# Optimization experiments

Hardware: AMD Instinct MI355X
Metric: run time of the kernel (lower is better)

## Reference

```python
import jax, jax.numpy as jnp
import numpy as np

BN_EPS = 1e-5


def setup_inputs() -> dict:
    key = jax.random.key(0)
    k1, k2, k3, k4 = jax.random.split(key, 4)
    B, H, W, C = 2, 256, 256, 256
    x = jax.random.normal(k1, (B, H, W, C), dtype=jnp.float32)
    # 1x1 conv weights (bias=False), randomly initialized each forward in the original
    w_down = jax.random.normal(k2, (16, C), dtype=jnp.float32) * (1.0 / np.sqrt(C))
    w_up = jax.random.normal(k3, (C, 16), dtype=jnp.float32) * (1.0 / np.sqrt(16))
    w_final = jax.random.normal(k4, (C, 2 * C), dtype=jnp.float32) * (1.0 / np.sqrt(2 * C))
    return {"x": x, "w_down": w_down, "w_up": w_up, "w_final": w_final}


def reference(x, w_down, w_up, w_final):
    # x: [B, H, W, C] -> NCHW
    x = jnp.transpose(x, (0, 3, 1, 2))  # [B, C, H, W]
    B, C, H, W = x.shape
    # fresh BatchNorm2d in training mode: batch stats, weight=1, bias=0
    mean = jnp.mean(x, axis=(0, 2, 3), keepdims=True)
    var = jnp.var(x, axis=(0, 2, 3), keepdims=True)  # biased variance
    xn = (x - mean) * jax.lax.rsqrt(var + BN_EPS)  # [B, C, H, W]
    # relu -> sigmoid
    a = jax.nn.sigmoid(jax.nn.relu(xn))
    # down-channel 1x1 conv: C -> 16
    y = jnp.einsum('oc,bchw->bohw', w_down, a)  # [B, 16, H, W]
    f = y.reshape(B, 16, H * W)  # flattened per-sample [16, HW]
    # channel self-attention; NOTE: source bug reuses Gram of sample 0 for sample 1
    G0 = f[0] @ f[0].T  # [16, 16]
    out0 = G0 @ f[0]    # [16, HW]
    out1 = G0 @ f[1]    # [16, HW]  (faithful to xcam4b = Dot(xcam3a, xcam1b))
    xcam4 = jnp.stack([out0, out1], axis=0).reshape(B, 16, H, W)
    # up-channel 1x1 conv: 16 -> C
    up = jnp.einsum('co,bohw->bchw', w_up, xcam4)  # [B, C, H, W]
    cat = jnp.concatenate([xn, up], axis=1)  # [B, 2C, H, W]
    # final down-channel 1x1 conv: 2C -> C
    out = jnp.einsum('oc,bchw->bohw', w_final, cat)  # [B, C, H, W]
    return out
```

## Files before the change

kernel.cpp:

```cpp
#include <hip/hip_runtime.h>
#include <stdint.h>

typedef __attribute__((ext_vector_type(8))) short bf16x8;
typedef __attribute__((ext_vector_type(4))) float f32x4;

#define CC 256
#define HWP 65536

__device__ __forceinline__ unsigned short f2bf(float f) {
    union { float f; unsigned int u; } v; v.f = f;
    unsigned int u = v.u;
    return (unsigned short)((u + 0x7fffu + ((u >> 16) & 1u)) >> 16);
}
__device__ __forceinline__ unsigned int f2bf2(float lo, float hi) {
    return (unsigned)f2bf(lo) | ((unsigned)f2bf(hi) << 16);
}
__device__ __forceinline__ float sigm_relu(float xn) {
    float xr = fmaxf(xn, 0.f);
    float e = __expf(-xr);
    return __builtin_amdgcn_rcpf(1.f + e);
}

__global__ __launch_bounds__(512, 8) void k1_part(const float* __restrict__ x,
                                                  float* __restrict__ part) {
    __shared__ float red[8][520];
    const int t = threadIdx.x, bid = blockIdx.x;
    const int c4 = (t & 63) * 4, po = t >> 6;
    const float* xp = x + ((size_t)(bid * 256 + po)) * CC + c4;
    f32x4 s = {0.f, 0.f, 0.f, 0.f}, q = {0.f, 0.f, 0.f, 0.f};
    #pragma unroll 8
    for (int p = 0; p < 32; ++p) {
        f32x4 v = *(const f32x4*)(xp + (size_t)p * 8 * CC);
        s += v; q += v * v;
    }
    *(f32x4*)&red[po][c4] = s;
    *(f32x4*)&red[po][256 + c4] = q;
    __syncthreads();
    float r = 0.f;
    #pragma unroll
    for (int po2 = 0; po2 < 8; ++po2) r += red[po2][t];
    part[bid * 512 + t] = r;
}

__global__ __launch_bounds__(256) void k2a_red(const float* __restrict__ part,
                                               float* __restrict__ p2) {
    int t = threadIdx.x, r = blockIdx.x;
    float s = 0.f, q = 0.f;
    #pragma unroll
    for (int i = 0; i < 16; ++i) {
        s += part[(size_t)(r * 16 + i) * 512 + t];
        q += part[(size_t)(r * 16 + i) * 512 + 256 + t];
    }
    p2[r * 512 + t] = s;
    p2[r * 512 + 256 + t] = q;
}

__global__ __launch_bounds__(256) void k2b_stats(const float* __restrict__ p2,
                                                 float* __restrict__ mg,
                                                 float* __restrict__ ig) {
    int c = threadIdx.x;
    float s = 0.f, q = 0.f;
    #pragma unroll
    for (int r = 0; r < 32; ++r) { s += p2[r * 512 + c]; q += p2[r * 512 + 256 + c]; }
    float mean = s * (1.f / 131072.f);
    float var  = q * (1.f / 131072.f) - mean * mean;
    mg[c] = mean;
    ig[c] = rsqrtf(var + 1e-5f);
}

__global__ __launch_bounds__(512) void k3_gram(const float* __restrict__ x,
                                               const float* __restrict__ wd,
                                               const float* __restrict__ mg,
                                               const float* __restrict__ ig,
                                               float* __restrict__ gpart) {
    __shared__ uint4 apack[2048];
    __shared__ float y_s[2][16][68];
    const int t = threadIdx.x;
    const int w = t >> 6, lm = t & 15, lk = (t >> 4) & 3;
    const int h = w & 1, ntile = w >> 1;
    uint4 wfrag[4];
    #pragma unroll
    for (int kt = 0; kt < 4; ++kt) {
        const int kbr = h * 16 + kt * 4 + lk;
        f32x4 wa = *(const f32x4*)(wd + lm * 256 + kbr * 8);
        f32x4 wb = *(const f32x4*)(wd + lm * 256 + kbr * 8 + 4);
        wfrag[kt] = (uint4){f2bf2(wa[0], wa[1]), f2bf2(wa[2], wa[3]),
                            f2bf2(wb[0], wb[1]), f2bf2(wb[2], wb[3])};
    }
    const int kb = t & 31, c0 = kb * 8, nb = t >> 5;
    f32x4 m0 = *(const f32x4*)(mg + c0), m1 = *(const f32x4*)(mg + c0 + 4);
    f32x4 i0 = *(const f32x4*)(ig + c0), i1 = *(const f32x4*)(ig + c0 + 4);
    const float mm[8] = {m0[0],m0[1],m0[2],m0[3],m1[0],m1[1],m1[2],m1[3]};
    const float ii[8] = {i0[0],i0[1],i0[2],i0[3],i1[0],i1[1],i1[2],i1[3]};
    const int o1 = t >> 4, o2 = t & 15;
    float g = 0.f;
    for (int st = 0; st < 4; ++st) {
        const float* xb = x + ((size_t)(blockIdx.x * 256 + st * 64 + nb)) * CC + c0;
        #pragma unroll
        for (int rep = 0; rep < 4; ++rep) {
            int n = rep * 16 + nb;
            const float* xp = xb + (size_t)rep * 16 * CC;
            f32x4 v0 = *(const f32x4*)xp;
            f32x4 v1 = *(const f32x4*)(xp + 4);
            float vv[8] = {v0[0],v0[1],v0[2],v0[3],v1[0],v1[1],v1[2],v1[3]};
            unsigned aw[4];
            #pragma unroll
            for (int hh = 0; hh < 4; ++hh) {
                float a0 = sigm_relu((vv[2*hh]   - mm[2*hh])   * ii[2*hh]);
                float a1 = sigm_relu((vv[2*hh+1] - mm[2*hh+1]) * ii[2*hh+1]);
                aw[hh] = f2bf2(a0, a1);
            }
            apack[kb * 64 + (n ^ kb)] = (uint4){aw[0], aw[1], aw[2], aw[3]};
        }
        __syncthreads();
        f32x4 accY = {0.f, 0.f, 0.f, 0.f};
        #pragma unroll
        for (int kt = 0; kt < 4; ++kt) {
            const int kbr = h * 16 + kt * 4 + lk;
            uint4 u = apack[kbr * 64 + ((ntile * 16 + lm) ^ kbr)];
            accY = __builtin_amdgcn_mfma_f32_16x16x32_bf16(*(bf16x8*)&wfrag[kt], *(bf16x8*)&u, accY, 0, 0, 0);
        }
        #pragma unroll
        for (int i = 0; i < 4; ++i) y_s[h][lk * 4 + i][ntile * 16 + lm] = accY[i];
        __syncthreads();
        if (t < 256) {
            #pragma unroll
            for (int p4 = 0; p4 < 16; ++p4) {
                f32x4 a0 = *(const f32x4*)&y_s[0][o1][p4 * 4];
                f32x4 a1 = *(const f32x4*)&y_s[1][o1][p4 * 4];
                f32x4 b0 = *(const f32x4*)&y_s[0][o2][p4 * 4];
                f32x4 b1 = *(const f32x4*)&y_s[1][o2][p4 * 4];
                f32x4 ya = a0 + a1, yb = b0 + b1;
                g += ya[0]*yb[0] + ya[1]*yb[1] + ya[2]*yb[2] + ya[3]*yb[3];
            }
        }
        __syncthreads();
    }
    if (t < 256) gpart[blockIdx.x * 256 + t] = g;
}

__global__ __launch_bounds__(256) void k4_R(const float* __restrict__ gpart,
                                            const float* __restrict__ wd,
                                            float* __restrict__ Rg) {
    __shared__ float G_s[256];
    const int t = threadIdx.x;
    float g = 0.f;
    #pragma unroll 8
    for (int i = 0; i < 256; ++i) g += gpart[i * 256 + t];
    G_s[t] = g;
    __syncthreads();
    #pragma unroll
    for (int o = 0; o < 16; ++o) {
        float r = 0.f;
        #pragma unroll
        for (int o2 = 0; o2 < 16; ++o2) r += G_s[o * 16 + o2] * wd[o2 * 256 + t];
        Rg[o * 256 + t] = r;
    }
}

__global__ __launch_bounds__(256) void k5_wcb(const float* __restrict__ wf,
                                              const float* __restrict__ wu,
                                              const float* __restrict__ Rg,
                                              unsigned short* __restrict__ wcb) {
    __shared__ float M_s[16][17];
    const int t = threadIdx.x;
    const int lr = t >> 4, j = t & 15;
    const int r = blockIdx.x * 16 + lr;
    const float* wfr = wf + (size_t)r * 512;
    float m = 0.f;
    for (int c = 0; c < 256; ++c) m += wfr[256 + c] * wu[c * 16 + j];
    M_s[lr][j] = m;
    __syncthreads();
    float Ml[16];
    #pragma unroll
    for (int o = 0; o < 16; ++o) Ml[o] = M_s[lr][o];
    unsigned short* wrow = wcb + (size_t)r * 512;
    for (int i = 0; i < 16; ++i) {
        int c = j + 16 * i;
        wrow[c] = f2bf(wfr[c]);
        float kv = 0.f;
        #pragma unroll
        for (int o = 0; o < 16; ++o) kv += Ml[o] * Rg[o * 256 + c];
        wrow[256 + c] = f2bf(kv);
    }
}

__global__ __launch_bounds__(512, 4) void k6_main(const float* __restrict__ x,
                                                  const unsigned short* __restrict__ wcb,
                                                  const float* __restrict__ mg,
                                                  const float* __restrict__ ig,
                                                  float* __restrict__ out) {
    __shared__ __align__(16) char smem[69632];
    uint4* zpack = (uint4*)smem;
    float* T = (float*)smem;
    const int t = threadIdx.x;
    const int tile = blockIdx.x;
    const int b = tile >> 10;
    const int pw = (tile & 1023) * 64;
    {
        const int kb = t & 31, c0 = kb * 8, nb = t >> 5;
        f32x4 m0 = *(const f32x4*)(mg + c0), m1 = *(const f32x4*)(mg + c0 + 4);
        f32x4 i0 = *(const f32x4*)(ig + c0), i1 = *(const f32x4*)(ig + c0 + 4);
        float mm[8] = {m0[0],m0[1],m0[2],m0[3],m1[0],m1[1],m1[2],m1[3]};
        float ii[8] = {i0[0],i0[1],i0[2],i0[3],i1[0],i1[1],i1[2],i1[3]};
        const float* xb = x + ((size_t)(b * HWP + pw + nb)) * CC + c0;
        #pragma unroll
        for (int rep = 0; rep < 4; ++rep) {
            int n = rep * 16 + nb;
            const float* xp = xb + (size_t)rep * 16 * CC;
            f32x4 v0 = *(const f32x4*)xp;
            f32x4 v1 = *(const f32x4*)(xp + 4);
            float vv[8] = {v0[0],v0[1],v0[2],v0[3],v1[0],v1[1],v1[2],v1[3]};
            unsigned xw[4], aw[4];
            #pragma unroll
            for (int hh = 0; hh < 4; ++hh) {
                float xn0 = (vv[2*hh]   - mm[2*hh])   * ii[2*hh];
                float xn1 = (vv[2*hh+1] - mm[2*hh+1]) * ii[2*hh+1];
                xw[hh] = f2bf2(xn0, xn1);
                aw[hh] = f2bf2(sigm_relu(xn0), sigm_relu(xn1));
            }
            zpack[kb * 64 + (n ^ kb)] = (uint4){xw[0], xw[1], xw[2], xw[3]};
            zpack[(kb + 32) * 64 + (n ^ (kb + 32))] = (uint4){aw[0], aw[1], aw[2], aw[3]};
        }
    }
    __syncthreads();
    const int w = t >> 6, lm = t & 15, lk = (t >> 4) & 3;
    const unsigned short* wrow = wcb + (size_t)(w * 32 + lm) * 512 + lk * 8;
    f32x4 acc[4][2];
    #pragma unroll
    for (int mt = 0; mt < 4; ++mt)
        #pragma unroll
        for (int nt = 0; nt < 2; ++nt) acc[mt][nt] = (f32x4){0.f, 0.f, 0.f, 0.f};
    #pragma unroll 4
    for (int kt = 0; kt < 16; ++kt) {
        const int kbr = kt * 4 + lk;
        bf16x8 zfr[4], wfr[2];
        #pragma unroll
        for (int mt = 0; mt < 4; ++mt) {
            uint4 u = zpack[kbr * 64 + ((mt * 16 + lm) ^ kbr)];
            zfr[mt] = *(bf16x8*)&u;
        }
        #pragma unroll
        for (int nt = 0; nt < 2; ++nt)
            wfr[nt] = *(const bf16x8*)(wrow + (size_t)nt * 16 * 512 + kt * 32);
        #pragma unroll
        for (int mt = 0; mt < 4; ++mt)
            #pragma unroll
            for (int nt = 0; nt < 2; ++nt)
                acc[mt][nt] = __builtin_amdgcn_mfma_f32_16x16x32_bf16(zfr[mt], wfr[nt], acc[mt][nt], 0, 0, 0);
    }
    __syncthreads();
    #pragma unroll
    for (int nt = 0; nt < 2; ++nt) {
        const int ch = w * 32 + nt * 16 + lm;
        #pragma unroll
        for (int mt = 0; mt < 4; ++mt)
            *(f32x4*)&T[ch * 68 + mt * 16 + lk * 4] = acc[mt][nt];
    }
    __syncthreads();
    {
        const int row0 = t >> 4, pxq = t & 15;
        float* ob = out + (size_t)b * 256 * HWP + pw + pxq * 4;
        #pragma unroll
        for (int j = 0; j < 8; ++j) {
            const int row = j * 32 + row0;
            f32x4 v = *(const f32x4*)&T[row * 68 + pxq * 4];
            __builtin_nontemporal_store(v, (f32x4*)(ob + (size_t)row * HWP));
        }
    }
}

extern "C" void kernel_launch(void* const* d_in, const int* in_sizes, int n_in,
                              void* d_out, int out_size, void* d_ws, size_t ws_size,
                              hipStream_t stream) {
    const float* x  = (const float*)d_in[0];
    const float* wd = (const float*)d_in[1];
    const float* wu = (const float*)d_in[2];
    const float* wf = (const float*)d_in[3];
    float* out = (float*)d_out;
    char* ws = (char*)d_ws;
    unsigned short* wcb = (unsigned short*)ws;
    float* part  = (float*)(ws + 262144);
    float* p2    = (float*)(ws + 1310720);
    float* mg    = (float*)(ws + 1376256);
    float* ig    = (float*)(ws + 1377280);
    float* gpart = (float*)(ws + 1378304);
    float* Rg    = (float*)(ws + 1640448);

    k1_part <<<dim3(512),  dim3(512), 0, stream>>>(x, part);
    k2a_red <<<dim3(32),   dim3(256), 0, stream>>>(part, p2);
    k2b_stats<<<dim3(1),   dim3(256), 0, stream>>>(p2, mg, ig);
    k3_gram <<<dim3(256),  dim3(512), 0, stream>>>(x, wd, mg, ig, gpart);
    k4_R    <<<dim3(1),    dim3(256), 0, stream>>>(gpart, wd, Rg);
    k5_wcb  <<<dim3(16),   dim3(256), 0, stream>>>(wf, wu, Rg, wcb);
    k6_main <<<dim3(2048), dim3(512), 0, stream>>>(x, wcb, mg, ig, out);
}
```

Before: 175.8 us.

## Fuse Gram-reduce into weight-combine kernel, store main output directly from MFMA accumulators

Merges the single-block R computation into the weight-combine kernel, so each of the 16 blocks redundantly reduces the Gram partials and keeps R in shared memory, which removes one launch. The main kernel drops the shared-memory transpose staging and writes MFMA accumulators straight to global with nontemporal stores. It also preloads all x vectors before converting them, remaps block indices to interleave tiles, and switches to the library bf16 conversion. The direct stores are narrower 64-byte row segments, and the fused kernel repeats the gpart reduction in every block.

Result: faster. 150.7 us (median of 3 runs) (-14.2%).

```diff
diff --git a/kernel.cpp b/kernel.cpp
--- a/kernel.cpp
+++ b/kernel.cpp
@@ -1,4 +1,5 @@
 #include <hip/hip_runtime.h>
+#include <hip/hip_bf16.h>
 #include <stdint.h>
 
 typedef __attribute__((ext_vector_type(8))) short bf16x8;
@@ -12,8 +13,11 @@
     unsigned int u = v.u;
     return (unsigned short)((u + 0x7fffu + ((u >> 16) & 1u)) >> 16);
 }
-__device__ __forceinline__ unsigned int f2bf2(float lo, float hi) {
-    return (unsigned)f2bf(lo) | ((unsigned)f2bf(hi) << 16);
+__device__ __forceinline__ unsigned int pk2(float lo, float hi) {
+    union { __hip_bfloat16 b; unsigned short s; } ul, uh;
+    ul.b = __float2bfloat16(lo);
+    uh.b = __float2bfloat16(hi);
+    return (unsigned)ul.s | ((unsigned)uh.s << 16);
 }
 __device__ __forceinline__ float sigm_relu(float xn) {
     float xr = fmaxf(xn, 0.f);
@@ -84,8 +88,8 @@
         const int kbr = h * 16 + kt * 4 + lk;
         f32x4 wa = *(const f32x4*)(wd + lm * 256 + kbr * 8);
         f32x4 wb = *(const f32x4*)(wd + lm * 256 + kbr * 8 + 4);
-        wfrag[kt] = (uint4){f2bf2(wa[0], wa[1]), f2bf2(wa[2], wa[3]),
-                            f2bf2(wb[0], wb[1]), f2bf2(wb[2], wb[3])};
+        wfrag[kt] = (uint4){pk2(wa[0], wa[1]), pk2(wa[2], wa[3]),
+                            pk2(wb[0], wb[1]), pk2(wb[2], wb[3])};
     }
     const int kb = t & 31, c0 = kb * 8, nb = t >> 5;
     f32x4 m0 = *(const f32x4*)(mg + c0), m1 = *(const f32x4*)(mg + c0 + 4);
@@ -108,7 +112,7 @@
             for (int hh = 0; hh < 4; ++hh) {
                 float a0 = sigm_relu((vv[2*hh]   - mm[2*hh])   * ii[2*hh]);
                 float a1 = sigm_relu((vv[2*hh+1] - mm[2*hh+1]) * ii[2*hh+1]);
-                aw[hh] = f2bf2(a0, a1);
+                aw[hh] = pk2(a0, a1);
             }
             apack[kb * 64 + (n ^ kb)] = (uint4){aw[0], aw[1], aw[2], aw[3]};
         }
@@ -139,10 +143,14 @@
     if (t < 256) gpart[blockIdx.x * 256 + t] = g;
 }
 
-__global__ __launch_bounds__(256) void k4_R(const float* __restrict__ gpart,
-                                            const float* __restrict__ wd,
-                                            float* __restrict__ Rg) {
+__global__ __launch_bounds__(256) void k45_wcb(const float* __restrict__ gpart,
+                                               const float* __restrict__ wd,
+                                               const float* __restrict__ wf,
+                                               const float* __restrict__ wu,
+                                               unsigned short* __restrict__ wcb) {
     __shared__ float G_s[256];
+    __shared__ float R_s[16][256];
+    __shared__ float M_s[16][17];
     const int t = threadIdx.x;
     float g = 0.f;
     #pragma unroll 8
@@ -154,16 +162,8 @@
         float r = 0.f;
         #pragma unroll
         for (int o2 = 0; o2 < 16; ++o2) r += G_s[o * 16 + o2] * wd[o2 * 256 + t];
-        Rg[o * 256 + t] = r;
-    }
-}
-
-__global__ __launch_bounds__(256) void k5_wcb(const float* __restrict__ wf,
-                                              const float* __restrict__ wu,
-                                              const float* __restrict__ Rg,
-                                              unsigned short* __restrict__ wcb) {
-    __shared__ float M_s[16][17];
-    const int t = threadIdx.x;
+        R_s[o][t] = r;
+    }
     const int lr = t >> 4, j = t & 15;
     const int r = blockIdx.x * 16 + lr;
     const float* wfr = wf + (size_t)r * 512;
@@ -180,7 +180,7 @@
         wrow[c] = f2bf(wfr[c]);
         float kv = 0.f;
         #pragma unroll
-        for (int o = 0; o < 16; ++o) kv += Ml[o] * Rg[o * 256 + c];
+        for (int o = 0; o < 16; ++o) kv += Ml[o] * R_s[o][c];
         wrow[256 + c] = f2bf(kv);
     }
 }
@@ -190,38 +190,38 @@
                                                   const float* __restrict__ mg,
                                                   const float* __restrict__ ig,
                                                   float* __restrict__ out) {
-    __shared__ __align__(16) char smem[69632];
-    uint4* zpack = (uint4*)smem;
-    float* T = (float*)smem;
+    __shared__ uint4 zpack[4096];
     const int t = threadIdx.x;
-    const int tile = blockIdx.x;
+    const int tile = (blockIdx.x & 7) * 256 + (blockIdx.x >> 3);
     const int b = tile >> 10;
     const int pw = (tile & 1023) * 64;
-    {
-        const int kb = t & 31, c0 = kb * 8, nb = t >> 5;
-        f32x4 m0 = *(const f32x4*)(mg + c0), m1 = *(const f32x4*)(mg + c0 + 4);
-        f32x4 i0 = *(const f32x4*)(ig + c0), i1 = *(const f32x4*)(ig + c0 + 4);
-        float mm[8] = {m0[0],m0[1],m0[2],m0[3],m1[0],m1[1],m1[2],m1[3]};
-        float ii[8] = {i0[0],i0[1],i0[2],i0[3],i1[0],i1[1],i1[2],i1[3]};
-        const float* xb = x + ((size_t)(b * HWP + pw + nb)) * CC + c0;
-        #pragma unroll
-        for (int rep = 0; rep < 4; ++rep) {
-            int n = rep * 16 + nb;
-            const float* xp = xb + (size_t)rep * 16 * CC;
-            f32x4 v0 = *(const f32x4*)xp;
-            f32x4 v1 = *(const f32x4*)(xp + 4);
-            float vv[8] = {v0[0],v0[1],v0[2],v0[3],v1[0],v1[1],v1[2],v1[3]};
-            unsigned xw[4], aw[4];
-            #pragma unroll
-            for (int hh = 0; hh < 4; ++hh) {
-                float xn0 = (vv[2*hh]   - mm[2*hh])   * ii[2*hh];
-                float xn1 = (vv[2*hh+1] - mm[2*hh+1]) * ii[2*hh+1];
-                xw[hh] = f2bf2(xn0, xn1);
-                aw[hh] = f2bf2(sigm_relu(xn0), sigm_relu(xn1));
-            }
-            zpack[kb * 64 + (n ^ kb)] = (uint4){xw[0], xw[1], xw[2], xw[3]};
-            zpack[(kb + 32) * 64 + (n ^ (kb + 32))] = (uint4){aw[0], aw[1], aw[2], aw[3]};
-        }
+    const int kb = t & 31, c0 = kb * 8, nb = t >> 5;
+    f32x4 m0 = *(const f32x4*)(mg + c0), m1 = *(const f32x4*)(mg + c0 + 4);
+    f32x4 i0 = *(const f32x4*)(ig + c0), i1 = *(const f32x4*)(ig + c0 + 4);
+    const float mm[8] = {m0[0],m0[1],m0[2],m0[3],m1[0],m1[1],m1[2],m1[3]};
+    const float ii[8] = {i0[0],i0[1],i0[2],i0[3],i1[0],i1[1],i1[2],i1[3]};
+    const float* xb = x + ((size_t)(b * HWP + pw + nb)) * CC + c0;
+    f32x4 v[8];
+    #pragma unroll
+    for (int rep = 0; rep < 4; ++rep) {
+        v[2 * rep]     = *(const f32x4*)(xb + (size_t)rep * 16 * CC);
+        v[2 * rep + 1] = *(const f32x4*)(xb + (size_t)rep * 16 * CC + 4);
+    }
+    #pragma unroll
+    for (int rep = 0; rep < 4; ++rep) {
+        const int px = rep * 16 + nb;
+        f32x4 v0 = v[2 * rep], v1 = v[2 * rep + 1];
+        float vv[8] = {v0[0],v0[1],v0[2],v0[3],v1[0],v1[1],v1[2],v1[3]};
+        unsigned xw[4], aw[4];
+        #pragma unroll
+        for (int hh = 0; hh < 4; ++hh) {
+            float xn0 = (vv[2*hh]   - mm[2*hh])   * ii[2*hh];
+            float xn1 = (vv[2*hh+1] - mm[2*hh+1]) * ii[2*hh+1];
+            xw[hh] = pk2(xn0, xn1);
+            aw[hh] = pk2(sigm_relu(xn0), sigm_relu(xn1));
+        }
+        zpack[kb * 64 + ((px ^ kb) & 63)] = (uint4){xw[0], xw[1], xw[2], xw[3]};
+        zpack[(kb + 32) * 64 + ((px ^ (kb + 32)) & 63)] = (uint4){aw[0], aw[1], aw[2], aw[3]};
     }
     __syncthreads();
     const int w = t >> 6, lm = t & 15, lk = (t >> 4) & 3;
@@ -237,7 +237,7 @@
         bf16x8 zfr[4], wfr[2];
         #pragma unroll
         for (int mt = 0; mt < 4; ++mt) {
-            uint4 u = zpack[kbr * 64 + ((mt * 16 + lm) ^ kbr)];
+            uint4 u = zpack[kbr * 64 + (((mt * 16 + lm) ^ kbr) & 63)];
             zfr[mt] = *(bf16x8*)&u;
         }
         #pragma unroll
@@ -249,24 +249,12 @@
             for (int nt = 0; nt < 2; ++nt)
                 acc[mt][nt] = __builtin_amdgcn_mfma_f32_16x16x32_bf16(zfr[mt], wfr[nt], acc[mt][nt], 0, 0, 0);
     }
-    __syncthreads();
     #pragma unroll
     for (int nt = 0; nt < 2; ++nt) {
-        const int ch = w * 32 + nt * 16 + lm;
+        float* ob = out + ((size_t)(b * 256 + w * 32 + nt * 16 + lm)) * HWP + pw + lk * 4;
         #pragma unroll
         for (int mt = 0; mt < 4; ++mt)
-            *(f32x4*)&T[ch * 68 + mt * 16 + lk * 4] = acc[mt][nt];
-    }
-    __syncthreads();
-    {
-        const int row0 = t >> 4, pxq = t & 15;
-        float* ob = out + (size_t)b * 256 * HWP + pw + pxq * 4;
-        #pragma unroll
-        for (int j = 0; j < 8; ++j) {
-            const int row = j * 32 + row0;
-            f32x4 v = *(const f32x4*)&T[row * 68 + pxq * 4];
-            __builtin_nontemporal_store(v, (f32x4*)(ob + (size_t)row * HWP));
-        }
+            __builtin_nontemporal_store(acc[mt][nt], (f32x4*)(ob + mt * 16));
     }
 }
 
@@ -285,13 +273,11 @@
     float* mg    = (float*)(ws + 1376256);
     float* ig    = (float*)(ws + 1377280);
     float* gpart = (float*)(ws + 1378304);
-    float* Rg    = (float*)(ws + 1640448);
 
     k1_part <<<dim3(512),  dim3(512), 0, stream>>>(x, part);
     k2a_red <<<dim3(32),   dim3(256), 0, stream>>>(part, p2);
     k2b_stats<<<dim3(1),   dim3(256), 0, stream>>>(p2, mg, ig);
     k3_gram <<<dim3(256),  dim3(512), 0, stream>>>(x, wd, mg, ig, gpart);
-    k4_R    <<<dim3(1),    dim3(256), 0, stream>>>(gpart, wd, Rg);
-    k5_wcb  <<<dim3(16),   dim3(256), 0, stream>>>(wf, wu, Rg, wcb);
+    k45_wcb <<<dim3(16),   dim3(256), 0, stream>>>(gpart, wd, wf, wu, wcb);
     k6_main <<<dim3(2048), dim3(512), 0, stream>>>(x, wcb, mg, ig, out);
 }
```
